# Performance work log

Measured on AMD Instinct MI355X. Metric: run time of the kernel, lower is better.

The kernel has to match this reference:

```python
import jax, jax.numpy as jnp
import numpy as np

NUM_GROUPS = 8
EPS = 1e-5


def group_norm(x, gamma, beta):
    # x: [B, C, H, W]
    B, C, H, W = x.shape
    xg = x.reshape(B, NUM_GROUPS, C // NUM_GROUPS, H, W)
    mean = xg.mean(axis=(2, 3, 4), keepdims=True)
    var = xg.var(axis=(2, 3, 4), keepdims=True)
    xn = ((xg - mean) * jax.lax.rsqrt(var + EPS)).reshape(B, C, H, W)
    return xn * gamma[None, :, None, None] + beta[None, :, None, None]


def conv1x1(x, w, b):
    # x: [B, C, H, W], w: [Cout, Cin], b: [Cout]
    return jnp.einsum('bchw,oc->bohw', x, w) + b[None, :, None, None]


def setup_inputs() -> dict:
    key = jax.random.key(0)
    ks = jax.random.split(key, 7)
    C = 128
    x = jax.random.normal(ks[0], (4, C, 64, 64), dtype=jnp.float32)
    norm_w = jnp.ones((C,), dtype=jnp.float32)
    norm_b = jnp.zeros((C,), dtype=jnp.float32)
    s = 1.0 / np.sqrt(C)
    qkv_w = jax.random.normal(ks[1], (3 * C, C), dtype=jnp.float32) * s
    qkv_b = jax.random.normal(ks[2], (3 * C,), dtype=jnp.float32) * 0.01
    proj_w = jax.random.normal(ks[3], (C, C), dtype=jnp.float32) * s
    proj_b = jax.random.normal(ks[4], (C,), dtype=jnp.float32) * 0.01
    return {"x": x, "norm_w": norm_w, "norm_b": norm_b,
            "qkv_w": qkv_w, "qkv_b": qkv_b,
            "proj_w": proj_w, "proj_b": proj_b}


def reference(x, norm_w, norm_b, qkv_w, qkv_b, proj_w, proj_b):
    B, C, H, W = x.shape
    qkv = conv1x1(group_norm(x, norm_w, norm_b), qkv_w, qkv_b)
    q, k, v = jnp.split(qkv, 3, axis=1)           # each [B, C, H, W]
    q = q.reshape(B, C, H * W).transpose(0, 2, 1)  # [B, HW, C]
    k = k.reshape(B, C, H * W)                     # [B, C, HW]
    v = v.reshape(B, C, H * W).transpose(0, 2, 1)  # [B, HW, C]
    scale = 1.0 / np.sqrt(C).astype(np.float32)
    attn = jax.nn.softmax(jnp.einsum('bnc,bcm->bnm', q, k) * scale, axis=-1)
    out = jnp.einsum('bnm,bmc->bnc', attn, v)      # [B, HW, C]
    out = out.transpose(0, 2, 1).reshape(B, C, H, W)
    return x + conv1x1(out, proj_w, proj_b)
```

## Files before the change

kernel.cpp:

```cpp
#include <hip/hip_runtime.h>

typedef unsigned short u16;
typedef unsigned int   u32;

#define HW 4096
#define NC 128

typedef __bf16 bf16x8 __attribute__((ext_vector_type(8)));
typedef float  f32x16 __attribute__((ext_vector_type(16)));

__device__ __forceinline__ bf16x8 as_bf8(uint4 u){
    union { uint4 u; bf16x8 b; } c; c.u = u; return c.b;
}
__device__ __forceinline__ u16 f2bf(float f){
    u32 u = __float_as_uint(f);
    return (u16)((u + 0x7fffu + ((u >> 16) & 1u)) >> 16);
}
__device__ __forceinline__ u32 pack2(float a, float b){
    return ((__float_as_uint(a) + 0x8000u) >> 16) | ((__float_as_uint(b) + 0x8000u) & 0xffff0000u);
}
__device__ __forceinline__ float bf_lo(u32 u){ return __uint_as_float(u << 16); }
__device__ __forceinline__ float bf_hi(u32 u){ return __uint_as_float(u & 0xffff0000u); }
__device__ __forceinline__ void unpack8(uint4 u, float* v){
    v[0]=bf_lo(u.x); v[1]=bf_hi(u.x); v[2]=bf_lo(u.y); v[3]=bf_hi(u.y);
    v[4]=bf_lo(u.z); v[5]=bf_hi(u.z); v[6]=bf_lo(u.w); v[7]=bf_hi(u.w);
}

__device__ __forceinline__ float exp2_hw(float x){ return __builtin_amdgcn_exp2f(x); }

__global__ __launch_bounds__(256) void gnw_kernel(const float* __restrict__ x,
                                                  float* __restrict__ stats,
                                                  const float* __restrict__ qkv_w,
                                                  const float* __restrict__ proj_w,
                                                  uint4* __restrict__ Wf,
                                                  uint4* __restrict__ Pf){
    if (blockIdx.x < 256){
        int bg = blockIdx.x >> 3, part = blockIdx.x & 7;
        const float4* p = (const float4*)(x + (size_t)bg * 65536 + part * 8192);
        float s = 0.f, ss = 0.f;
        #pragma unroll
        for (int i = 0; i < 8; i++){
            float4 u = p[threadIdx.x + i*256];
            s  += u.x + u.y + u.z + u.w;
            ss += u.x*u.x + u.y*u.y + u.z*u.z + u.w*u.w;
        }
        #pragma unroll
        for (int off = 32; off > 0; off >>= 1){
            s  += __shfl_xor(s,  off);
            ss += __shfl_xor(ss, off);
        }
        __shared__ float rs[4], rss[4];
        int wid = threadIdx.x >> 6;
        if ((threadIdx.x & 63) == 0){ rs[wid] = s; rss[wid] = ss; }
        __syncthreads();
        if (threadIdx.x == 0){
            stats[bg*16 + part*2]     = rs[0]+rs[1]+rs[2]+rs[3];
            stats[bg*16 + part*2 + 1] = rss[0]+rss[1]+rss[2]+rss[3];
        }
    } else {
        int id = (blockIdx.x - 256)*256 + threadIdx.x;
        const float* src; uint4* dst; int fi;
        if (id < 6144){ src = qkv_w; dst = Wf; fi = id; }
        else          { src = proj_w; dst = Pf; fi = id - 6144; }
        int l = fi & 63, ks = (fi >> 6) & 7, ob = fi >> 9;
        int o = ob*32 + (l & 31);
        int c = ks*16 + ((l >> 5) << 3);
        const float* s = src + o*128 + c;
        dst[fi] = make_uint4(pack2(s[0],s[1]), pack2(s[2],s[3]), pack2(s[4],s[5]), pack2(s[6],s[7]));
    }
}

__global__ __launch_bounds__(256) void qkv_kernel(const float* __restrict__ x,
                                                  const float* __restrict__ stats,
                                                  const float* __restrict__ gamma,
                                                  const float* __restrict__ beta,
                                                  const uint4* __restrict__ Wf,
                                                  const float* __restrict__ bias,
                                                  uint4* __restrict__ Qf,
                                                  uint4* __restrict__ Kf,
                                                  uint4* __restrict__ Vf){
    __shared__ float gaL[128], beL[128], biasL[384];
    int b = blockIdx.x >> 7, tokblk = blockIdx.x & 127;
    int t = threadIdx.x, lane = t & 63, wv = t >> 6;
    if (t < 128){
        int g = t >> 4;
        float S = 0.f, SS = 0.f;
        #pragma unroll
        for (int p = 0; p < 8; p++){
            S  += stats[(b*8 + g)*16 + p*2];
            SS += stats[(b*8 + g)*16 + p*2 + 1];
        }
        float mean = S * (1.f/65536.f);
        float rstd = rsqrtf(SS * (1.f/65536.f) - mean*mean + 1e-5f);
        float ga = gamma[t] * rstd;
        gaL[t] = ga; beL[t] = beta[t] - mean*ga;
    }
    if (t < 192){ biasL[t] = bias[t]; biasL[t+192] = bias[t+192]; }
    __syncthreads();

    int h = lane >> 5, tl = lane & 31;
    uint4 xf[8];
    const float* xb = x + (size_t)b*128*HW + tokblk*32 + tl;
    #pragma unroll
    for (int ks = 0; ks < 8; ks++){
        int c0 = ks*16 + h*8;
        float4 g0 = *(float4*)&gaL[c0], g1 = *(float4*)&gaL[c0+4];
        float4 e0 = *(float4*)&beL[c0], e1 = *(float4*)&beL[c0+4];
        float v[8];
        #pragma unroll
        for (int j = 0; j < 8; j++) v[j] = xb[(size_t)(c0+j)*HW];
        v[0] = fmaf(v[0], g0.x, e0.x); v[1] = fmaf(v[1], g0.y, e0.y);
        v[2] = fmaf(v[2], g0.z, e0.z); v[3] = fmaf(v[3], g0.w, e0.w);
        v[4] = fmaf(v[4], g1.x, e1.x); v[5] = fmaf(v[5], g1.y, e1.y);
        v[6] = fmaf(v[6], g1.z, e1.z); v[7] = fmaf(v[7], g1.w, e1.w);
        xf[ks] = make_uint4(pack2(v[0],v[1]), pack2(v[2],v[3]), pack2(v[4],v[5]), pack2(v[6],v[7]));
    }

    bool up = (lane >= 32);
    #pragma unroll
    for (int i = 0; i < 3; i++){
        int ob = wv*3 + i;
        uint4 wf[8];
        #pragma unroll
        for (int ks = 0; ks < 8; ks++) wf[ks] = Wf[(ob*8 + ks)*64 + lane];
        f32x16 D;
        #pragma unroll
        for (int r = 0; r < 16; r++) D[r] = 0.f;
        if (ob < 8){
            #pragma unroll
            for (int ks = 0; ks < 8; ks++)
                D = __builtin_amdgcn_mfma_f32_32x32x16_bf16(as_bf8(wf[ks]), as_bf8(xf[ks]), D, 0,0,0);
            #pragma unroll
            for (int r = 0; r < 16; r++)
                D[r] += biasL[ob*32 + (r&3) + 8*(r>>2) + 4*h];
            u32 pk[8], xch[8];
            #pragma unroll
            for (int j = 0; j < 8; j++) pk[j] = pack2(D[2*j], D[2*j+1]);
            #pragma unroll
            for (int j = 0; j < 8; j++) xch[j] = __shfl_xor(pk[j], 32);
            uint4 F0 = up ? make_uint4(xch[2],xch[3],pk[2],pk[3]) : make_uint4(pk[0],pk[1],xch[0],xch[1]);
            uint4 F1 = up ? make_uint4(xch[6],xch[7],pk[6],pk[7]) : make_uint4(pk[4],pk[5],xch[4],xch[5]);
            uint4* dst = (ob < 4) ? Qf : Kf;
            int obl = ob & 3;
            size_t base = (((size_t)b*128 + tokblk)*8 + obl*2)*64 + lane;
            dst[base] = F0; dst[base + 64] = F1;
        } else {
            #pragma unroll
            for (int ks = 0; ks < 8; ks++)
                D = __builtin_amdgcn_mfma_f32_32x32x16_bf16(as_bf8(xf[ks]), as_bf8(wf[ks]), D, 0,0,0);
            int nb = ob - 8;
            float vb = biasL[256 + nb*32 + tl];
            #pragma unroll
            for (int r = 0; r < 16; r++) D[r] += vb;
            u32 pk[8], xch[8];
            #pragma unroll
            for (int j = 0; j < 8; j++) pk[j] = pack2(D[2*j], D[2*j+1]);
            #pragma unroll
            for (int j = 0; j < 8; j++) xch[j] = __shfl_xor(pk[j], 32);
            uint4 F0 = up ? make_uint4(xch[2],xch[3],pk[2],pk[3]) : make_uint4(pk[0],pk[1],xch[0],xch[1]);
            uint4 F1 = up ? make_uint4(xch[6],xch[7],pk[6],pk[7]) : make_uint4(pk[4],pk[5],xch[4],xch[5]);
            int it = tokblk >> 1, t2 = tokblk & 1;
            size_t base = ((((size_t)b*64 + it)*4 + nb)*4 + t2*2)*64 + lane;
            Vf[base] = F0; Vf[base + 64] = F1;
        }
    }
}

__global__ __launch_bounds__(256, 2) void attn_kernel(const uint4* __restrict__ Qf,
                                                      const uint4* __restrict__ Kf,
                                                      const uint4* __restrict__ Vf,
                                                      uint4* __restrict__ Opart,
                                                      float* __restrict__ lsum){
    __shared__ float fsm[8192];
    __shared__ float lred[64];
    int pair = blockIdx.x & 7, qx = blockIdx.x >> 3;
    int b = pair >> 1, ksp = pair & 1;
    int t = threadIdx.x, lane = t & 63, wv = t >> 6;
    int qh = wv >> 1, kh = wv & 1;
    const float SC2 = 0.12751744361402804f;
    const float B2  = -11.541560327111707f;

    uint4 qf[8];
    const uint4* qptr = Qf + (((size_t)b*128 + qx*2 + qh)*8)*64 + lane;
    #pragma unroll
    for (int ks = 0; ks < 8; ks++) qf[ks] = qptr[ks*64];

    f32x16 O[4];
    #pragma unroll
    for (int nb = 0; nb < 4; nb++)
        #pragma unroll
        for (int r = 0; r < 16; r++) O[nb][r] = 0.f;
    float l_i = 0.f;

    const uint4* kgw = Kf + (((size_t)b*128 + ksp*64)*8)*64 + (kh<<9) + lane;
    const uint4* vgw = Vf + (((size_t)b*64  + ksp*32)*16)*64 + (kh<<7) + lane;

    uint4 kf[8], vf[8];
    #pragma unroll
    for (int ks = 0; ks < 8; ks++) kf[ks] = kgw[ks*64];
    #pragma unroll
    for (int nb = 0; nb < 4; nb++){
        vf[nb*2]   = vgw[nb*256];
        vf[nb*2+1] = vgw[nb*256 + 64];
    }

    for (int it = 0; it < 32; it++){
        f32x16 Sa, Sb;
        #pragma unroll
        for (int r = 0; r < 16; r++){ Sa[r] = 0.f; Sb[r] = 0.f; }
        #pragma unroll
        for (int ks = 0; ks < 4; ks++)
            Sa = __builtin_amdgcn_mfma_f32_32x32x16_bf16(as_bf8(kf[ks]), as_bf8(qf[ks]), Sa, 0,0,0);
        #pragma unroll
        for (int ks = 4; ks < 8; ks++)
            Sb = __builtin_amdgcn_mfma_f32_32x32x16_bf16(as_bf8(kf[ks]), as_bf8(qf[ks]), Sb, 0,0,0);
        #pragma unroll
        for (int r = 0; r < 16; r++) Sa[r] += Sb[r];

        if (it < 31){
            const uint4* kn = kgw + (it+1)*1024;
            #pragma unroll
            for (int ks = 0; ks < 8; ks++) kf[ks] = kn[ks*64];
        }

        float psum = 0.f;
        u32 pk[8];
        #pragma unroll
        for (int q = 0; q < 4; q++){
            float e0 = exp2_hw(__fmaf_rn(Sa[q*4+0], SC2, B2));
            float e1 = exp2_hw(__fmaf_rn(Sa[q*4+1], SC2, B2));
            float e2 = exp2_hw(__fmaf_rn(Sa[q*4+2], SC2, B2));
            float e3 = exp2_hw(__fmaf_rn(Sa[q*4+3], SC2, B2));
            psum += (e0+e1)+(e2+e3);
            pk[2*q] = pack2(e0,e1); pk[2*q+1] = pack2(e2,e3);
        }
        psum += __shfl_xor(psum, 32);
        l_i += psum;

        u32 xch[8];
        #pragma unroll
        for (int i = 0; i < 8; i++) xch[i] = __shfl_xor(pk[i], 32);
        bool up = (lane >= 32);
        uint4 fr0 = up ? make_uint4(xch[2],xch[3],pk[2],pk[3]) : make_uint4(pk[0],pk[1],xch[0],xch[1]);
        uint4 fr1 = up ? make_uint4(xch[6],xch[7],pk[6],pk[7]) : make_uint4(pk[4],pk[5],xch[4],xch[5]);

        #pragma unroll
        for (int nb = 0; nb < 4; nb++){
            O[nb] = __builtin_amdgcn_mfma_f32_32x32x16_bf16(as_bf8(vf[nb*2]),   as_bf8(fr0), O[nb], 0,0,0);
            O[nb] = __builtin_amdgcn_mfma_f32_32x32x16_bf16(as_bf8(vf[nb*2+1]), as_bf8(fr1), O[nb], 0,0,0);
        }

        if (it < 31){
            const uint4* vn = vgw + (it+1)*1024;
            #pragma unroll
            for (int nb = 0; nb < 4; nb++){
                vf[nb*2]   = vn[nb*256];
                vf[nb*2+1] = vn[nb*256 + 64];
            }
        }
    }

    if (kh == 1){
        #pragma unroll
        for (int nb = 0; nb < 4; nb++)
            #pragma unroll
            for (int r = 0; r < 16; r++)
                fsm[((qh*4+nb)*16 + r)*64 + lane] = O[nb][r];
        if (lane < 32) lred[qh*32 + lane] = l_i;
    }
    __syncthreads();
    if (kh == 0){
        float lt = l_i + lred[qh*32 + (lane & 31)];
        if (lane < 32) lsum[((size_t)(ksp*4 + b))*HW + (qx*2+qh)*32 + lane] = lt;
        bool up = (lane >= 32);
        uint4* oc = Opart + (size_t)ksp*262144 + (((size_t)b*128 + qx*2 + qh)*8)*64 + lane;
        #pragma unroll
        for (int nb = 0; nb < 4; nb++){
            #pragma unroll
            for (int r = 0; r < 16; r++) O[nb][r] += fsm[((qh*4+nb)*16 + r)*64 + lane];
            u32 pk[8], xch[8];
            #pragma unroll
            for (int j = 0; j < 8; j++) pk[j] = pack2(O[nb][2*j], O[nb][2*j+1]);
            #pragma unroll
            for (int j = 0; j < 8; j++) xch[j] = __shfl_xor(pk[j], 32);
            uint4 F0 = up ? make_uint4(xch[2],xch[3],pk[2],pk[3]) : make_uint4(pk[0],pk[1],xch[0],xch[1]);
            uint4 F1 = up ? make_uint4(xch[6],xch[7],pk[6],pk[7]) : make_uint4(pk[4],pk[5],xch[4],xch[5]);
            oc[(nb*2)*64]     = F0;
            oc[(nb*2 + 1)*64] = F1;
        }
    }
}

__global__ __launch_bounds__(256) void proj_kernel(const uint4* __restrict__ Op,
                                                   const float* __restrict__ lsum,
                                                   const uint4* __restrict__ Pf,
                                                   const float* __restrict__ bias,
                                                   const float* __restrict__ x,
                                                   float* __restrict__ out){
    __shared__ float biasL[128];
    int t = threadIdx.x, lane = t & 63, wv = t >> 6;
    if (t < 128) biasL[t] = bias[t];
    __syncthreads();
    int b = blockIdx.x >> 6, tk = blockIdx.x & 63;
    int tokb2 = wv & 1, obh = wv >> 1;
    int tokblk = tk*2 + tokb2;
    int h = lane >> 5, tl = lane & 31;

    int rowg = b*HW + tokblk*32 + tl;
    float inv = 1.f / (lsum[rowg] + lsum[16384 + rowg]);
    const uint4* c0p = Op + (((size_t)b*128 + tokblk)*8)*64 + lane;
    uint4 af[8];
    #pragma unroll
    for (int ks = 0; ks < 8; ks++){
        uint4 u0 = c0p[ks*64];
        uint4 u1 = c0p[262144 + ks*64];
        float v0[8], v1[8];
        unpack8(u0, v0); unpack8(u1, v1);
        u32 q[4];
        #pragma unroll
        for (int j = 0; j < 4; j++)
            q[j] = pack2((v0[2*j] + v1[2*j]) * inv, (v0[2*j+1] + v1[2*j+1]) * inv);
        af[ks] = make_uint4(q[0], q[1], q[2], q[3]);
    }

    #pragma unroll
    for (int i = 0; i < 2; i++){
        int ob = obh*2 + i;
        uint4 pf[8];
        #pragma unroll
        for (int ks = 0; ks < 8; ks++) pf[ks] = Pf[(ob*8 + ks)*64 + lane];
        f32x16 D;
        #pragma unroll
        for (int r = 0; r < 16; r++) D[r] = 0.f;
        #pragma unroll
        for (int ks = 0; ks < 8; ks++)
            D = __builtin_amdgcn_mfma_f32_32x32x16_bf16(as_bf8(pf[ks]), as_bf8(af[ks]), D, 0,0,0);
        #pragma unroll
        for (int r = 0; r < 16; r++){
            int o = ob*32 + (r&3) + 8*(r>>2) + 4*h;
            size_t gi = ((size_t)b*128 + o)*HW + tokblk*32 + tl;
            out[gi] = x[gi] + biasL[o] + D[r];
        }
    }
}

extern "C" void kernel_launch(void* const* d_in, const int* in_sizes, int n_in,
                              void* d_out, int out_size, void* d_ws, size_t ws_size,
                              hipStream_t stream){
    const float* x      = (const float*)d_in[0];
    const float* norm_w = (const float*)d_in[1];
    const float* norm_b = (const float*)d_in[2];
    const float* qkv_w  = (const float*)d_in[3];
    const float* qkv_b  = (const float*)d_in[4];
    const float* proj_w = (const float*)d_in[5];
    const float* proj_b = (const float*)d_in[6];
    float* out = (float*)d_out;

    char* w = (char*)d_ws;
    float* stats = (float*)w;
    uint4* Qf = (uint4*)(w + 2048);
    uint4* Kf = (uint4*)(w + 2048 + 4194304);
    uint4* Vf = (uint4*)(w + 2048 + 8388608);
    float* lsum = (float*)(w + 2048 + 12582912);
    uint4* Wf = (uint4*)(w + 2048 + 12582912 + 131072);
    uint4* Pf = (uint4*)(w + 2048 + 12582912 + 131072 + 98304);
    uint4* Opart = (uint4*)d_out;

    gnw_kernel<<<288, 256, 0, stream>>>(x, stats, qkv_w, proj_w, Wf, Pf);
    qkv_kernel<<<512, 256, 0, stream>>>(x, stats, norm_w, norm_b, Wf, qkv_b, Qf, Kf, Vf);
    attn_kernel<<<512, 256, 0, stream>>>(Qf, Kf, Vf, Opart, lsum);
    proj_kernel<<<256, 256, 0, stream>>>(Opart, lsum, Pf, proj_b, x, out);
}
```

Before: 134.6 us.

## Software-pipeline QK^T one tile ahead of softmax and PV, add MFMA priority

Restructures the attention loop so the QK^T MFMAs for the next K tile are issued before the exp/pack/shuffle softmax work on the current tile. K loads are prefetched two tiles ahead. This is meant to let the MFMA pipe overlap with the VALU exp and the cross-lane shuffles. It also wraps the MFMA blocks in s_setprio to favour issuing matrix instructions across waves. The cost is another 16-register score accumulator and more live registers, which could lower occupancy or cause spills.

```diff
diff --git a/kernel.cpp b/kernel.cpp
--- a/kernel.cpp
+++ b/kernel.cpp
@@ -204,21 +204,44 @@
         vf[nb*2+1] = vgw[nb*256 + 64];
     }
 
+    f32x16 Scur;
+    {
+        f32x16 Sa, Sb;
+        #pragma unroll
+        for (int r = 0; r < 16; r++){ Sa[r] = 0.f; Sb[r] = 0.f; }
+        __builtin_amdgcn_s_setprio(1);
+        #pragma unroll
+        for (int ks = 0; ks < 4; ks++)
+            Sa = __builtin_amdgcn_mfma_f32_32x32x16_bf16(as_bf8(kf[ks]), as_bf8(qf[ks]), Sa, 0,0,0);
+        #pragma unroll
+        for (int ks = 4; ks < 8; ks++)
+            Sb = __builtin_amdgcn_mfma_f32_32x32x16_bf16(as_bf8(kf[ks]), as_bf8(qf[ks]), Sb, 0,0,0);
+        __builtin_amdgcn_s_setprio(0);
+        {
+            const uint4* kn = kgw + 1024;
+            #pragma unroll
+            for (int ks = 0; ks < 8; ks++) kf[ks] = kn[ks*64];
+        }
+        #pragma unroll
+        for (int r = 0; r < 16; r++) Scur[r] = Sa[r] + Sb[r];
+    }
+
     for (int it = 0; it < 32; it++){
         f32x16 Sa, Sb;
         #pragma unroll
         for (int r = 0; r < 16; r++){ Sa[r] = 0.f; Sb[r] = 0.f; }
-        #pragma unroll
-        for (int ks = 0; ks < 4; ks++)
-            Sa = __builtin_amdgcn_mfma_f32_32x32x16_bf16(as_bf8(kf[ks]), as_bf8(qf[ks]), Sa, 0,0,0);
-        #pragma unroll
-        for (int ks = 4; ks < 8; ks++)
-            Sb = __builtin_amdgcn_mfma_f32_32x32x16_bf16(as_bf8(kf[ks]), as_bf8(qf[ks]), Sb, 0,0,0);
-        #pragma unroll
-        for (int r = 0; r < 16; r++) Sa[r] += Sb[r];
-
         if (it < 31){
-            const uint4* kn = kgw + (it+1)*1024;
+            __builtin_amdgcn_s_setprio(1);
+            #pragma unroll
+            for (int ks = 0; ks < 4; ks++)
+                Sa = __builtin_amdgcn_mfma_f32_32x32x16_bf16(as_bf8(kf[ks]), as_bf8(qf[ks]), Sa, 0,0,0);
+            #pragma unroll
+            for (int ks = 4; ks < 8; ks++)
+                Sb = __builtin_amdgcn_mfma_f32_32x32x16_bf16(as_bf8(kf[ks]), as_bf8(qf[ks]), Sb, 0,0,0);
+            __builtin_amdgcn_s_setprio(0);
+        }
+        if (it < 30){
+            const uint4* kn = kgw + (it+2)*1024;
             #pragma unroll
             for (int ks = 0; ks < 8; ks++) kf[ks] = kn[ks*64];
         }
@@ -227,10 +250,10 @@
         u32 pk[8];
         #pragma unroll
         for (int q = 0; q < 4; q++){
-            float e0 = exp2_hw(__fmaf_rn(Sa[q*4+0], SC2, B2));
-            float e1 = exp2_hw(__fmaf_rn(Sa[q*4+1], SC2, B2));
-            float e2 = exp2_hw(__fmaf_rn(Sa[q*4+2], SC2, B2));
-            float e3 = exp2_hw(__fmaf_rn(Sa[q*4+3], SC2, B2));
+            float e0 = exp2_hw(__fmaf_rn(Scur[q*4+0], SC2, B2));
+            float e1 = exp2_hw(__fmaf_rn(Scur[q*4+1], SC2, B2));
+            float e2 = exp2_hw(__fmaf_rn(Scur[q*4+2], SC2, B2));
+            float e3 = exp2_hw(__fmaf_rn(Scur[q*4+3], SC2, B2));
             psum += (e0+e1)+(e2+e3);
             pk[2*q] = pack2(e0,e1); pk[2*q+1] = pack2(e2,e3);
         }
@@ -244,11 +267,13 @@
         uint4 fr0 = up ? make_uint4(xch[2],xch[3],pk[2],pk[3]) : make_uint4(pk[0],pk[1],xch[0],xch[1]);
         uint4 fr1 = up ? make_uint4(xch[6],xch[7],pk[6],pk[7]) : make_uint4(pk[4],pk[5],xch[4],xch[5]);
 
+        __builtin_amdgcn_s_setprio(1);
         #pragma unroll
         for (int nb = 0; nb < 4; nb++){
             O[nb] = __builtin_amdgcn_mfma_f32_32x32x16_bf16(as_bf8(vf[nb*2]),   as_bf8(fr0), O[nb], 0,0,0);
             O[nb] = __builtin_amdgcn_mfma_f32_32x32x16_bf16(as_bf8(vf[nb*2+1]), as_bf8(fr1), O[nb], 0,0,0);
         }
+        __builtin_amdgcn_s_setprio(0);
 
         if (it < 31){
             const uint4* vn = vgw + (it+1)*1024;
@@ -258,6 +283,9 @@
                 vf[nb*2+1] = vn[nb*256 + 64];
             }
         }
+
+        #pragma unroll
+        for (int r = 0; r < 16; r++) Scur[r] = Sa[r] + Sb[r];
     }
 
     if (kh == 1){
```

Result: no change. 136.9 us (+1.7%).
